# Kernel optimization log

Hardware: AMD Instinct MI355X
Metric: run time of the kernel (lower is better)

## Reference

```python
import jax, jax.numpy as jnp
import numpy as np

N_NODES = 50000
N_EDGES = 800000
H = 128
D = 128
N_LAYERS = 4
N_GRAPHS = 128
NODE_VOCAB = 32
EDGE_VOCAB = 8
BN_EPS = 1e-5


def _bn(h, g, b):
    # BatchNorm1d, training-mode statistics (biased variance), as in the torch module
    m = h.mean(axis=0)
    v = ((h - m) ** 2).mean(axis=0)
    return (h - m) * jax.lax.rsqrt(v + BN_EPS) * g + b


def _gine(x, src, dst, e, eps_l):
    # GINEConv: message = ReLU(x_src + edge_attr), sum-aggregate at dst
    msg = jax.nn.relu(x[src] + e)                      # [E, H]
    aggr = jax.ops.segment_sum(msg, dst, num_segments=N_NODES)
    return (1.0 + eps_l) * x + aggr


def _forward(x_ids, edge_index, batch, edge_attr,
             node_emb, edge_emb, eps,
             init_W1, init_b1, init_g1, init_be1, init_W2, init_b2, init_g2, init_be2,
             mp_W1, mp_g1, mp_be1, mp_W2, mp_g2, mp_be2,
             l1_W1, l1_g1, l1_b1, l1_W2, l1_g2, l1_b2,
             l2_W1, l2_g1, l2_b1, l2_W2, l2_g2, l2_b2,
             fin_W):
    src, dst = edge_index[0], edge_index[1]
    x = node_emb[x_ids]                                # [N, H]
    e = edge_emb[edge_attr]                            # [E, H]
    # initialization conv (Linear layers WITH bias)
    h = _gine(x, src, dst, e, eps[0])
    h = jax.nn.relu(_bn(h @ init_W1 + init_b1, init_g1, init_be1))
    x = jax.nn.relu(_bn(h @ init_W2 + init_b2, init_g2, init_be2))
    # message-passing layers (Linear layers WITHOUT bias)
    for i in range(N_LAYERS):
        h = _gine(x, src, dst, e, eps[1 + i])
        h = jax.nn.relu(_bn(h @ mp_W1[i], mp_g1[i], mp_be1[i]))
        x = jax.nn.relu(_bn(h @ mp_W2[i], mp_g2[i], mp_be2[i]))
    # readout: global_add_pool
    g = jax.ops.segment_sum(x, batch, num_segments=N_GRAPHS)   # [G, H]
    # lin1 (outer F.relu is idempotent; dropout = identity in eval)
    h = jax.nn.relu(_bn(g @ l1_W1, l1_g1, l1_b1))
    h = jax.nn.relu(_bn(h @ l1_W2, l1_g2, l1_b2))
    # lin2
    h = jax.nn.relu(_bn(h @ l2_W1, l2_g1, l2_b1))
    h = jax.nn.relu(_bn(h @ l2_W2, l2_g2, l2_b2))
    return h @ fin_W                                   # [G, 1]


def setup_inputs() -> dict:
    key = jax.random.key(0)
    ks = jax.random.split(key, 20)
    s = 1.0 / np.sqrt(H)
    rn = lambda k, shp, sc: jax.random.normal(k, shp, dtype=jnp.float32) * sc
    return {
        "x_ids": jax.random.randint(ks[0], (N_NODES,), 0, NODE_VOCAB),
        "edge_index": jax.random.randint(ks[1], (2, N_EDGES), 0, N_NODES),
        "batch": jnp.sort(jax.random.randint(ks[2], (N_NODES,), 0, N_GRAPHS)),
        "edge_attr": jax.random.randint(ks[14], (N_EDGES,), 0, EDGE_VOCAB),
        "node_emb": rn(ks[3], (NODE_VOCAB, H), 0.05),
        "edge_emb": rn(ks[4], (EDGE_VOCAB, H), 0.05),
        "eps": jnp.zeros((N_LAYERS + 1,), jnp.float32),
        "init_W1": rn(ks[5], (H, D), s), "init_b1": jnp.zeros((D,)),
        "init_g1": jnp.ones((D,)), "init_be1": jnp.zeros((D,)),
        "init_W2": rn(ks[6], (D, H), s), "init_b2": jnp.zeros((H,)),
        "init_g2": jnp.ones((H,)), "init_be2": jnp.zeros((H,)),
        "mp_W1": rn(ks[7], (N_LAYERS, H, D), s),
        "mp_g1": jnp.ones((N_LAYERS, D)), "mp_be1": jnp.zeros((N_LAYERS, D)),
        "mp_W2": rn(ks[8], (N_LAYERS, D, H), s),
        "mp_g2": jnp.ones((N_LAYERS, H)), "mp_be2": jnp.zeros((N_LAYERS, H)),
        "l1_W1": rn(ks[9], (H, D), s), "l1_g1": jnp.ones((D,)), "l1_b1": jnp.zeros((D,)),
        "l1_W2": rn(ks[10], (D, D), s), "l1_g2": jnp.ones((D,)), "l1_b2": jnp.zeros((D,)),
        "l2_W1": rn(ks[11], (D, D), s), "l2_g1": jnp.ones((D,)), "l2_b1": jnp.zeros((D,)),
        "l2_W2": rn(ks[12], (D, H), s), "l2_g2": jnp.ones((H,)), "l2_b2": jnp.zeros((H,)),
        "fin_W": rn(ks[13], (H, 1), s),
    }


def reference(x_ids, edge_index, batch, edge_attr,
              node_emb, edge_emb, eps,
              init_W1, init_b1, init_g1, init_be1, init_W2, init_b2, init_g2, init_be2,
              mp_W1, mp_g1, mp_be1, mp_W2, mp_g2, mp_be2,
              l1_W1, l1_g1, l1_b1, l1_W2, l1_g2, l1_b2,
              l2_W1, l2_g1, l2_b1, l2_W2, l2_g2, l2_b2,
              fin_W):
    return _forward(x_ids, edge_index, batch, edge_attr,
                    node_emb, edge_emb, eps,
                    init_W1, init_b1, init_g1, init_be1, init_W2, init_b2, init_g2, init_be2,
                    mp_W1, mp_g1, mp_be1, mp_W2, mp_g2, mp_be2,
                    l1_W1, l1_g1, l1_b1, l1_W2, l1_g2, l1_b2,
                    l2_W1, l2_g1, l2_b1, l2_W2, l2_g2, l2_b2,
                    fin_W)
```

## Files before the change

kernel.cpp:

```cpp
#include <hip/hip_runtime.h>

#define NN 50000
#define NE 800000
#define NG 128
#define HD 128
#define NL 4
#define BN_EPS 1e-5f
#define REP 32
#define WP 136
#define NB 392
#define EPB 4096

typedef __attribute__((ext_vector_type(8))) short bf16x8;
typedef __attribute__((ext_vector_type(4))) float f32x4;

__device__ __forceinline__ unsigned short f2bf(float f) {
    unsigned u = __float_as_uint(f);
    u += 0x7FFFu + ((u >> 16) & 1u);
    return (unsigned short)(u >> 16);
}
__device__ __forceinline__ float bfval(unsigned short h) { return __uint_as_float((unsigned)h << 16); }
__device__ __forceinline__ float bflo(unsigned u) { return __uint_as_float(u << 16); }
__device__ __forceinline__ float bfhi(unsigned u) { return __uint_as_float(u & 0xFFFF0000u); }

__device__ __forceinline__ void split2(float a, float b, unsigned& hi, unsigned& lo) {
    unsigned ua = __float_as_uint(a), ub = __float_as_uint(b);
    hi = (ua >> 16) | (ub & 0xFFFF0000u);
    float ra = a - __uint_as_float(ua & 0xFFFF0000u);
    float rb = b - __uint_as_float(ub & 0xFFFF0000u);
    lo = (unsigned)f2bf(ra) | ((unsigned)f2bf(rb) << 16);
}
__device__ __forceinline__ unsigned pack2(float a, float b) {
    return (unsigned)f2bf(a) | ((unsigned)f2bf(b) << 16);
}

__device__ __forceinline__ void bn_pre(const float* SQbase,
                                       const float* gam, const float* bet,
                                       float inv_cnt, int t, float* scs, float* shs) {
    if (gam == nullptr) { scs[t] = 1.f; shs[t] = 0.f; return; }
    float s = 0.f, q = 0.f;
#pragma unroll
    for (int r = 0; r < REP; r++) {
        s += SQbase[r * 256 + t];
        q += SQbase[r * 256 + 128 + t];
    }
    float m = s * inv_cnt;
    float var = fmaxf(fmaf(q, inv_cnt, -m * m), 0.f);
    float inv = rsqrtf(var + BN_EPS);
    float sc = gam[t] * inv;
    scs[t] = sc;
    shs[t] = fmaf(-m, sc, bet[t]);
}

__global__ __launch_bounds__(256) void setup_kernel(const int* __restrict__ ids,
                                                    const float* __restrict__ emb,
                                                    unsigned short* __restrict__ Yb,
                                                    const float* __restrict__ iw1,
                                                    const float* __restrict__ iw2,
                                                    const float* __restrict__ mw1,
                                                    const float* __restrict__ mw2,
                                                    unsigned short* __restrict__ Wh,
                                                    unsigned short* __restrict__ Wl,
                                                    const int* __restrict__ dst,
                                                    int* __restrict__ deg) {
    int b = blockIdx.x, t = threadIdx.x;
    if (b < 3125) {
        int i = b * 256 + t;
        if (i < NN * 16) {
            int node = i >> 4, g = i & 15;
            int id = ids[node];
            const float* p = emb + (size_t)id * HD + 8 * g;
            float4 a = *(const float4*)p;
            float4 bb = *(const float4*)(p + 4);
            uint4 o;
            o.x = pack2(a.x, a.y); o.y = pack2(a.z, a.w);
            o.z = pack2(bb.x, bb.y); o.w = pack2(bb.z, bb.w);
            *(uint4*)(Yb + (size_t)node * HD + 8 * g) = o;
        }
    } else if (b < 3765) {
        int i = (b - 3125) * 256 + t;
        if (i < 163840) {
            int seg = i >> 14, loc = i & 16383;
            float v;
            if (seg == 0)      v = iw1[loc];
            else if (seg == 1) v = iw2[loc];
            else if (seg < 6)  v = mw1[(seg - 2) * 16384 + loc];
            else               v = mw2[(seg - 6) * 16384 + loc];
            int k = loc >> 7, n = loc & 127;
            unsigned short h = f2bf(v);
            float r = v - bfval(h);
            Wh[seg * 16384 + n * 128 + k] = h;
            Wl[seg * 16384 + n * 128 + k] = f2bf(r);
        }
    } else {
        int e = (b - 3765) * 256 + t;
        if (e < NE) atomicAdd(&deg[dst[e]], 1);
    }
}

__global__ __launch_bounds__(256) void ybn_kernel(const float* __restrict__ X,
                                                  const float* __restrict__ SQin,
                                                  const float* __restrict__ gam,
                                                  const float* __restrict__ bet,
                                                  unsigned short* __restrict__ Yb) {
    __shared__ float scs[HD], shs[HD];
    int t = threadIdx.x;
    if (t < HD) bn_pre(SQin, gam, bet, 1.f / NN, t, scs, shs);
    __syncthreads();
    int row = blockIdx.x * 16 + (t >> 4);
    int c8 = (t & 15) * 8;
    if (row < NN) {
        const float* p = X + (size_t)row * HD + c8;
        float4 v0 = *(const float4*)p;
        float4 v1 = *(const float4*)(p + 4);
        float4 s0 = *(const float4*)&scs[c8], s1 = *(const float4*)&scs[c8 + 4];
        float4 h0 = *(const float4*)&shs[c8], h1 = *(const float4*)&shs[c8 + 4];
        float f0 = fmaxf(fmaf(v0.x, s0.x, h0.x), 0.f), f1 = fmaxf(fmaf(v0.y, s0.y, h0.y), 0.f);
        float f2 = fmaxf(fmaf(v0.z, s0.z, h0.z), 0.f), f3 = fmaxf(fmaf(v0.w, s0.w, h0.w), 0.f);
        float f4 = fmaxf(fmaf(v1.x, s1.x, h1.x), 0.f), f5 = fmaxf(fmaf(v1.y, s1.y, h1.y), 0.f);
        float f6 = fmaxf(fmaf(v1.z, s1.z, h1.z), 0.f), f7 = fmaxf(fmaf(v1.w, s1.w, h1.w), 0.f);
        uint4 o;
        o.x = pack2(f0, f1); o.y = pack2(f2, f3);
        o.z = pack2(f4, f5); o.w = pack2(f6, f7);
        *(uint4*)(Yb + (size_t)row * HD + c8) = o;
    }
}

__global__ __launch_bounds__(1024) void scan1_kernel(const int* __restrict__ deg,
                                                     int* __restrict__ rowptr,
                                                     int* __restrict__ blockSum) {
    __shared__ int s[1024];
    int b = blockIdx.x, t = threadIdx.x;
    int i = b * 1024 + t;
    int v = (i < NN) ? deg[i] : 0;
    s[t] = v;
    __syncthreads();
    for (int off = 1; off < 1024; off <<= 1) {
        int u = (t >= off) ? s[t - off] : 0;
        __syncthreads();
        s[t] += u;
        __syncthreads();
    }
    if (i < NN) rowptr[i] = s[t] - v;
    if (t == 1023) blockSum[b] = s[1023];
}

__global__ __launch_bounds__(64) void scan2_kernel(const int* __restrict__ blockSum,
                                                   int* __restrict__ blockOff,
                                                   int* __restrict__ rowptr, int nblocks) {
    int t = threadIdx.x;
    int orig = (t < nblocks) ? blockSum[t] : 0;
    int v = orig;
    for (int off = 1; off < 64; off <<= 1) {
        int u = __shfl_up(v, off, 64);
        if (t >= off) v += u;
    }
    if (t < nblocks) blockOff[t] = v - orig;
    if (t == nblocks - 1) rowptr[NN] = v;
}

__global__ __launch_bounds__(1024) void scan3_kernel(int* __restrict__ rowptr,
                                                     int* __restrict__ cursor,
                                                     const int* __restrict__ blockOff,
                                                     int* __restrict__ bucketCursor) {
    int b = blockIdx.x, t = threadIdx.x;
    int i = b * 1024 + t;
    if (i < NN) {
        int r = rowptr[i] + blockOff[b];
        rowptr[i] = r;
        cursor[i] = r;
        if ((i & 127) == 0) bucketCursor[i >> 7] = r;
    }
}

__global__ __launch_bounds__(256) void bin_kernel(const int* __restrict__ src,
                                                  const int* __restrict__ dst,
                                                  const int* __restrict__ attr,
                                                  int* __restrict__ bucketCursor,
                                                  uint2* __restrict__ ebuf) {
    __shared__ int cnt[512];
    __shared__ int sc[512], sc2[512];
    __shared__ int base[512];
    __shared__ int garr[NB];
    __shared__ int wof[NB];
    __shared__ uint2 stage[EPB];
    int t = threadIdx.x;
    int e0 = blockIdx.x * EPB;
    for (int i = t; i < 512; i += 256) cnt[i] = 0;
    __syncthreads();
    int myb[16]; unsigned myv[16]; int myd[16];
#pragma unroll
    for (int j = 0; j < 16; j++) {
        int e = e0 + t + j * 256;
        if (e < NE) {
            int d = dst[e];
            myd[j] = d;
            myv[j] = (unsigned)src[e] | ((unsigned)attr[e] << 16);
            myb[j] = d >> 7;
            atomicAdd(&cnt[myb[j]], 1);
        } else myb[j] = -1;
    }
    __syncthreads();
    for (int k = t; k < 512; k += 256) sc[k] = cnt[k];
    __syncthreads();
    int* sp = sc; int* dp = sc2;
    for (int off = 1; off < 512; off <<= 1) {
        for (int k = t; k < 512; k += 256) dp[k] = sp[k] + (k >= off ? sp[k - off] : 0);
        __syncthreads();
        int* tmp = sp; sp = dp; dp = tmp;
    }
    for (int k = t; k < 512; k += 256) base[k] = sp[k] - cnt[k];
    int total = sp[511];
    __syncthreads();
    for (int b = t; b < NB; b += 256) {
        wof[b] = 0;
        if (cnt[b] > 0) garr[b] = atomicAdd(&bucketCursor[b], cnt[b]);
    }
    __syncthreads();
#pragma unroll
    for (int j = 0; j < 16; j++) {
        if (myb[j] >= 0) {
            int slot = base[myb[j]] + atomicAdd(&wof[myb[j]], 1);
            stage[slot] = make_uint2(myv[j], (unsigned)myd[j]);
        }
    }
    __syncthreads();
    for (int i = t; i < total; i += 256) {
        uint2 u = stage[i];
        int b = (int)(u.y >> 7);
        ebuf[garr[b] + (i - base[b])] = u;
    }
}

__global__ __launch_bounds__(256) void place_kernel(const uint2* __restrict__ ebuf,
                                                    const int* __restrict__ rowptr,
                                                    int* __restrict__ cursor,
                                                    unsigned* __restrict__ csr) {
    int b = blockIdx.x;
    int n0 = b * 128;
    int n1 = n0 + 128; if (n1 > NN) n1 = NN;
    int es = rowptr[n0], ee = rowptr[n1];
    for (int i = es + threadIdx.x; i < ee; i += 256) {
        uint2 u = ebuf[i];
        int pos = atomicAdd(&cursor[u.y], 1);
        csr[pos] = u.x;
    }
}

__device__ __forceinline__ void gine_acc(const unsigned short* __restrict__ Yb,
                                         const float* __restrict__ elds,
                                         unsigned p, int cq, float mask, float* a) {
    uint4 q = *(const uint4*)(Yb + (size_t)(p & 0xFFFFu) * HD + 8 * cq);
    const float* ep = elds + (p >> 16) * HD + 8 * cq;
    float4 e0 = *(const float4*)ep;
    float4 e1 = *(const float4*)(ep + 4);
    a[0] += mask * fmaxf(bflo(q.x) + e0.x, 0.f);
    a[1] += mask * fmaxf(bfhi(q.x) + e0.y, 0.f);
    a[2] += mask * fmaxf(bflo(q.y) + e0.z, 0.f);
    a[3] += mask * fmaxf(bfhi(q.y) + e0.w, 0.f);
    a[4] += mask * fmaxf(bflo(q.z) + e1.x, 0.f);
    a[5] += mask * fmaxf(bfhi(q.z) + e1.y, 0.f);
    a[6] += mask * fmaxf(bflo(q.w) + e1.z, 0.f);
    a[7] += mask * fmaxf(bfhi(q.w) + e1.w, 0.f);
}

__global__ __launch_bounds__(256) void conv_kernel(const unsigned short* __restrict__ Yb,
                                                   const int* __restrict__ rowptr,
                                                   const unsigned* __restrict__ csr,
                                                   const float* __restrict__ edge_emb,
                                                   const float* __restrict__ eps, int layer,
                                                   unsigned short* __restrict__ Ah,
                                                   unsigned short* __restrict__ Al) {
    __shared__ float elds[8 * HD];
    int t = threadIdx.x;
    ((float4*)elds)[t] = ((const float4*)edge_emb)[t];
    __syncthreads();
    int wave = t >> 6, lane = t & 63;
    int node = blockIdx.x * 4 + wave;
    if (node >= NN) return;
    int sub = lane >> 4, cq = lane & 15;
    int lo = rowptr[node], hi = rowptr[node + 1];
    float a[8];
#pragma unroll
    for (int i = 0; i < 8; i++) a[i] = 0.f;
    for (int base = lo; base < hi; base += 64) {
        unsigned pl = 0;
        int cnt = hi - base; if (cnt > 64) cnt = 64;
        if (base + lane < hi) pl = csr[base + lane];
        int j = 0;
        for (; j + 16 <= cnt; j += 16) {
            unsigned pa = __shfl(pl, j + sub, 64);
            unsigned pb = __shfl(pl, j + 4 + sub, 64);
            unsigned pc = __shfl(pl, j + 8 + sub, 64);
            unsigned pd = __shfl(pl, j + 12 + sub, 64);
            gine_acc(Yb, elds, pa, cq, 1.f, a);
            gine_acc(Yb, elds, pb, cq, 1.f, a);
            gine_acc(Yb, elds, pc, cq, 1.f, a);
            gine_acc(Yb, elds, pd, cq, 1.f, a);
        }
        for (; j + 8 <= cnt; j += 8) {
            unsigned pa = __shfl(pl, j + sub, 64);
            unsigned pb = __shfl(pl, j + 4 + sub, 64);
            gine_acc(Yb, elds, pa, cq, 1.f, a);
            gine_acc(Yb, elds, pb, cq, 1.f, a);
        }
        for (; j < cnt; j += 4) {
            int je = j + sub;
            bool val = (je < cnt);
            unsigned p = __shfl(pl, val ? je : j, 64);
            gine_acc(Yb, elds, p, cq, val ? 1.f : 0.f, a);
        }
    }
#pragma unroll
    for (int i = 0; i < 8; i++) {
        a[i] += __shfl_xor(a[i], 16, 64);
        a[i] += __shfl_xor(a[i], 32, 64);
    }
    if (sub == 0) {
        float g = 1.f + eps[layer];
        uint4 q = *(const uint4*)(Yb + (size_t)node * HD + 8 * cq);
        float o0 = fmaf(g, bflo(q.x), a[0]), o1 = fmaf(g, bfhi(q.x), a[1]);
        float o2 = fmaf(g, bflo(q.y), a[2]), o3 = fmaf(g, bfhi(q.y), a[3]);
        float o4 = fmaf(g, bflo(q.z), a[4]), o5 = fmaf(g, bfhi(q.z), a[5]);
        float o6 = fmaf(g, bflo(q.w), a[6]), o7 = fmaf(g, bfhi(q.w), a[7]);
        uint4 H, L;
        split2(o0, o1, H.x, L.x);
        split2(o2, o3, H.y, L.y);
        split2(o4, o5, H.z, L.z);
        split2(o6, o7, H.w, L.w);
        *(uint4*)(Ah + (size_t)node * HD + 8 * cq) = H;
        *(uint4*)(Al + (size_t)node * HD + 8 * cq) = L;
    }
}

__global__ __launch_bounds__(256) void mm_mfma_pre(const unsigned short* __restrict__ Ah,
                                                   const unsigned short* __restrict__ Al,
                                                   const unsigned short* __restrict__ Wh,
                                                   const unsigned short* __restrict__ Wl,
                                                   const float* __restrict__ bias,
                                                   float* __restrict__ out,
                                                   float* __restrict__ SQout) {
    __shared__ unsigned short WhS[128 * WP];
    __shared__ unsigned short WlS[128 * WP];
    int t = threadIdx.x;
    int rowblk = blockIdx.x;
#pragma unroll
    for (int i = 0; i < 8; i++) {
        int idx = t + i * 256;
        int col = idx >> 4, kk = (idx & 15) * 8;
        *(uint4*)(WhS + col * WP + kk) = *(const uint4*)(Wh + (size_t)col * HD + kk);
        *(uint4*)(WlS + col * WP + kk) = *(const uint4*)(Wl + (size_t)col * HD + kk);
    }
    __syncthreads();
    int w = t >> 6, lane = t & 63;
    int quad = lane >> 4, nl = lane & 15;
    int row0 = rowblk * 128 + w * 32;
    int rA0 = row0 + nl, rA1 = row0 + 16 + nl;
    bool ok0 = rA0 < NN, ok1 = rA1 < NN;
    f32x4 acc[16];
#pragma unroll
    for (int i = 0; i < 16; i++) acc[i] = (f32x4){0.f, 0.f, 0.f, 0.f};
#pragma unroll
    for (int kc = 0; kc < 4; kc++) {
        int k0 = kc * 32 + quad * 8;
        bf16x8 a0h = ok0 ? *(const bf16x8*)(Ah + (size_t)rA0 * HD + k0) : (bf16x8)0;
        bf16x8 a0l = ok0 ? *(const bf16x8*)(Al + (size_t)rA0 * HD + k0) : (bf16x8)0;
        bf16x8 a1h = ok1 ? *(const bf16x8*)(Ah + (size_t)rA1 * HD + k0) : (bf16x8)0;
        bf16x8 a1l = ok1 ? *(const bf16x8*)(Al + (size_t)rA1 * HD + k0) : (bf16x8)0;
#pragma unroll
        for (int c = 0; c < 8; c++) {
            int wof = (c * 16 + nl) * WP + k0;
            bf16x8 bh = *(const bf16x8*)(WhS + wof);
            bf16x8 bl = *(const bf16x8*)(WlS + wof);
            acc[c] = __builtin_amdgcn_mfma_f32_16x16x32_bf16(a0h, bh, acc[c], 0, 0, 0);
            acc[c] = __builtin_amdgcn_mfma_f32_16x16x32_bf16(a0l, bh, acc[c], 0, 0, 0);
            acc[c] = __builtin_amdgcn_mfma_f32_16x16x32_bf16(a0h, bl, acc[c], 0, 0, 0);
            acc[8 + c] = __builtin_amdgcn_mfma_f32_16x16x32_bf16(a1h, bh, acc[8 + c], 0, 0, 0);
            acc[8 + c] = __builtin_amdgcn_mfma_f32_16x16x32_bf16(a1l, bh, acc[8 + c], 0, 0, 0);
            acc[8 + c] = __builtin_amdgcn_mfma_f32_16x16x32_bf16(a1h, bl, acc[8 + c], 0, 0, 0);
        }
    }
    int rep = (blockIdx.x & (REP - 1)) * 256;
#pragma unroll
    for (int h = 0; h < 2; h++) {
        int baserow = row0 + h * 16 + quad * 4;
#pragma unroll
        for (int c = 0; c < 8; c++) {
            int col = c * 16 + nl;
            float bv = bias ? bias[col] : 0.f;
            f32x4 v = acc[h * 8 + c];
            float s = 0.f, qq = 0.f;
#pragma unroll
            for (int r = 0; r < 4; r++) {
                int grow = baserow + r;
                float val = v[r] + bv;
                if (grow < NN) {
                    out[(size_t)grow * HD + col] = val;
                    s += val;
                    qq += val * val;
                }
            }
            s += __shfl_xor(s, 16, 64);  s += __shfl_xor(s, 32, 64);
            qq += __shfl_xor(qq, 16, 64); qq += __shfl_xor(qq, 32, 64);
            if (quad == 0) {
                atomicAdd(&SQout[rep + col], s);
                atomicAdd(&SQout[rep + 128 + col], qq);
            }
        }
    }
}

__global__ __launch_bounds__(256) void mm_mfma_act(const float* __restrict__ A,
                                                   const unsigned short* __restrict__ Wh,
                                                   const unsigned short* __restrict__ Wl,
                                                   const float* __restrict__ bias,
                                                   const float* __restrict__ SQin,
                                                   const float* __restrict__ gam,
                                                   const float* __restrict__ bet,
                                                   float* __restrict__ out,
                                                   float* __restrict__ SQout) {
    __shared__ unsigned short WhS[128 * WP];
    __shared__ unsigned short WlS[128 * WP];
    __shared__ float scs[HD], shs[HD];
    int t = threadIdx.x;
    int rowblk = blockIdx.x;
    if (t < HD) bn_pre(SQin, gam, bet, 1.f / NN, t, scs, shs);
#pragma unroll
    for (int i = 0; i < 8; i++) {
        int idx = t + i * 256;
        int col = idx >> 4, kk = (idx & 15) * 8;
        *(uint4*)(WhS + col * WP + kk) = *(const uint4*)(Wh + (size_t)col * HD + kk);
        *(uint4*)(WlS + col * WP + kk) = *(const uint4*)(Wl + (size_t)col * HD + kk);
    }
    __syncthreads();
    int w = t >> 6, lane = t & 63;
    int quad = lane >> 4, nl = lane & 15;
    int row0 = rowblk * 128 + w * 32;
    int rA0 = row0 + nl, rA1 = row0 + 16 + nl;
    bool ok0 = rA0 < NN, ok1 = rA1 < NN;
    f32x4 acc[16];
#pragma unroll
    for (int i = 0; i < 16; i++) acc[i] = (f32x4){0.f, 0.f, 0.f, 0.f};
#pragma unroll
    for (int kc = 0; kc < 4; kc++) {
        int k0 = kc * 32 + quad * 8;
        float4 s0 = *(const float4*)&scs[k0], s1 = *(const float4*)&scs[k0 + 4];
        float4 t0 = *(const float4*)&shs[k0], t1 = *(const float4*)&shs[k0 + 4];
        bf16x8 a0h, a0l, a1h, a1l;
        {
            float4 v0 = ok0 ? *(const float4*)(A + (size_t)rA0 * HD + k0) : make_float4(0, 0, 0, 0);
            float4 v1 = ok0 ? *(const float4*)(A + (size_t)rA0 * HD + k0 + 4) : make_float4(0, 0, 0, 0);
            float f0 = fmaxf(fmaf(v0.x, s0.x, t0.x), 0.f), f1 = fmaxf(fmaf(v0.y, s0.y, t0.y), 0.f);
            float f2 = fmaxf(fmaf(v0.z, s0.z, t0.z), 0.f), f3 = fmaxf(fmaf(v0.w, s0.w, t0.w), 0.f);
            float f4 = fmaxf(fmaf(v1.x, s1.x, t1.x), 0.f), f5 = fmaxf(fmaf(v1.y, s1.y, t1.y), 0.f);
            float f6 = fmaxf(fmaf(v1.z, s1.z, t1.z), 0.f), f7 = fmaxf(fmaf(v1.w, s1.w, t1.w), 0.f);
            if (!ok0) { f0 = f1 = f2 = f3 = f4 = f5 = f6 = f7 = 0.f; }
            unsigned h0, h1, h2, h3, l0, l1, l2, l3;
            split2(f0, f1, h0, l0); split2(f2, f3, h1, l1);
            split2(f4, f5, h2, l2); split2(f6, f7, h3, l3);
            a0h = __builtin_bit_cast(bf16x8, make_uint4(h0, h1, h2, h3));
            a0l = __builtin_bit_cast(bf16x8, make_uint4(l0, l1, l2, l3));
        }
        {
            float4 v0 = ok1 ? *(const float4*)(A + (size_t)rA1 * HD + k0) : make_float4(0, 0, 0, 0);
            float4 v1 = ok1 ? *(const float4*)(A + (size_t)rA1 * HD + k0 + 4) : make_float4(0, 0, 0, 0);
            float f0 = fmaxf(fmaf(v0.x, s0.x, t0.x), 0.f), f1 = fmaxf(fmaf(v0.y, s0.y, t0.y), 0.f);
            float f2 = fmaxf(fmaf(v0.z, s0.z, t0.z), 0.f), f3 = fmaxf(fmaf(v0.w, s0.w, t0.w), 0.f);
            float f4 = fmaxf(fmaf(v1.x, s1.x, t1.x), 0.f), f5 = fmaxf(fmaf(v1.y, s1.y, t1.y), 0.f);
            float f6 = fmaxf(fmaf(v1.z, s1.z, t1.z), 0.f), f7 = fmaxf(fmaf(v1.w, s1.w, t1.w), 0.f);
            if (!ok1) { f0 = f1 = f2 = f3 = f4 = f5 = f6 = f7 = 0.f; }
            unsigned h0, h1, h2, h3, l0, l1, l2, l3;
            split2(f0, f1, h0, l0); split2(f2, f3, h1, l1);
            split2(f4, f5, h2, l2); split2(f6, f7, h3, l3);
            a1h = __builtin_bit_cast(bf16x8, make_uint4(h0, h1, h2, h3));
            a1l = __builtin_bit_cast(bf16x8, make_uint4(l0, l1, l2, l3));
        }
#pragma unroll
        for (int c = 0; c < 8; c++) {
            int wof = (c * 16 + nl) * WP + k0;
            bf16x8 bh = *(const bf16x8*)(WhS + wof);
            bf16x8 bl = *(const bf16x8*)(WlS + wof);
            acc[c] = __builtin_amdgcn_mfma_f32_16x16x32_bf16(a0h, bh, acc[c], 0, 0, 0);
            acc[c] = __builtin_amdgcn_mfma_f32_16x16x32_bf16(a0l, bh, acc[c], 0, 0, 0);
            acc[c] = __builtin_amdgcn_mfma_f32_16x16x32_bf16(a0h, bl, acc[c], 0, 0, 0);
            acc[8 + c] = __builtin_amdgcn_mfma_f32_16x16x32_bf16(a1h, bh, acc[8 + c], 0, 0, 0);
            acc[8 + c] = __builtin_amdgcn_mfma_f32_16x16x32_bf16(a1l, bh, acc[8 + c], 0, 0, 0);
            acc[8 + c] = __builtin_amdgcn_mfma_f32_16x16x32_bf16(a1h, bl, acc[8 + c], 0, 0, 0);
        }
    }
    int rep = (blockIdx.x & (REP - 1)) * 256;
#pragma unroll
    for (int h = 0; h < 2; h++) {
        int baserow = row0 + h * 16 + quad * 4;
#pragma unroll
        for (int c = 0; c < 8; c++) {
            int col = c * 16 + nl;
            float bv = bias ? bias[col] : 0.f;
            f32x4 v = acc[h * 8 + c];
            float s = 0.f, qq = 0.f;
#pragma unroll
            for (int r = 0; r < 4; r++) {
                int grow = baserow + r;
                float val = v[r] + bv;
                if (grow < NN) {
                    out[(size_t)grow * HD + col] = val;
                    s += val;
                    qq += val * val;
                }
            }
            s += __shfl_xor(s, 16, 64);  s += __shfl_xor(s, 32, 64);
            qq += __shfl_xor(qq, 16, 64); qq += __shfl_xor(qq, 32, 64);
            if (quad == 0) {
                atomicAdd(&SQout[rep + col], s);
                atomicAdd(&SQout[rep + 128 + col], qq);
            }
        }
    }
}

__global__ __launch_bounds__(256) void readout_kernel(const float* __restrict__ x,
                                                      const int* __restrict__ batch,
                                                      const float* __restrict__ SQin,
                                                      const float* __restrict__ gam,
                                                      const float* __restrict__ bet,
                                                      float* __restrict__ gout) {
    __shared__ int bat[256];
    __shared__ float scs[HD], shs[HD];
    int t = threadIdx.x;
    int rq = t >> 5, cq = t & 31;
    int r0 = blockIdx.x * 256;
    int i = r0 + t;
    bat[t] = (i < NN) ? batch[i] : -1;
    if (t < HD) bn_pre(SQin, gam, bet, 1.f / NN, t, scs, shs);
    __syncthreads();
    float4 s4 = *(const float4*)&scs[4 * cq];
    float4 h4 = *(const float4*)&shs[4 * cq];
    float4 acc = make_float4(0.f, 0.f, 0.f, 0.f);
    int gcur = -1;
    for (int j = rq; j < 256; j += 8) {
        int r = r0 + j;
        if (r >= NN) break;
        int g = bat[j];
        if (g != gcur) {
            if (gcur >= 0) {
                atomicAdd(&gout[(size_t)gcur * HD + 4 * cq + 0], acc.x);
                atomicAdd(&gout[(size_t)gcur * HD + 4 * cq + 1], acc.y);
                atomicAdd(&gout[(size_t)gcur * HD + 4 * cq + 2], acc.z);
                atomicAdd(&gout[(size_t)gcur * HD + 4 * cq + 3], acc.w);
            }
            acc = make_float4(0.f, 0.f, 0.f, 0.f);
            gcur = g;
        }
        float4 v = *(const float4*)(x + (size_t)r * HD + 4 * cq);
        acc.x += fmaxf(fmaf(v.x, s4.x, h4.x), 0.f);
        acc.y += fmaxf(fmaf(v.y, s4.y, h4.y), 0.f);
        acc.z += fmaxf(fmaf(v.z, s4.z, h4.z), 0.f);
        acc.w += fmaxf(fmaf(v.w, s4.w, h4.w), 0.f);
    }
    if (gcur >= 0) {
        atomicAdd(&gout[(size_t)gcur * HD + 4 * cq + 0], acc.x);
        atomicAdd(&gout[(size_t)gcur * HD + 4 * cq + 1], acc.y);
        atomicAdd(&gout[(size_t)gcur * HD + 4 * cq + 2], acc.z);
        atomicAdd(&gout[(size_t)gcur * HD + 4 * cq + 3], acc.w);
    }
}

__global__ __launch_bounds__(256) void head_fused(const float* __restrict__ Gp,
                                                  const float* __restrict__ Wa,
                                                  const float* __restrict__ Wb,
                                                  const float* __restrict__ Wc,
                                                  const float* __restrict__ Wd,
                                                  const float* __restrict__ g0,
                                                  const float* __restrict__ b0,
                                                  const float* __restrict__ g1,
                                                  const float* __restrict__ b1,
                                                  const float* __restrict__ g2,
                                                  const float* __restrict__ b2,
                                                  const float* __restrict__ g3,
                                                  const float* __restrict__ b3,
                                                  const float* __restrict__ finW,
                                                  float* __restrict__ out) {
    const int AP = 132;
    __shared__ float A_lds[128 * AP];
    __shared__ unsigned short WhS[128 * WP];
    __shared__ unsigned short WlS[128 * WP];
    __shared__ float colS[HD], colQ[HD], scs[HD], shs[HD];
    int t = threadIdx.x;
    if (t < HD) { colS[t] = 0.f; colQ[t] = 0.f; scs[t] = 1.f; shs[t] = 0.f; }
#pragma unroll
    for (int i = 0; i < 16; i++) {
        int idx = t + i * 256;
        int r = idx >> 5, cq = (idx & 31) * 4;
        *(float4*)&A_lds[r * AP + cq] = *(const float4*)(Gp + (size_t)r * HD + cq);
    }
    int w = t >> 6, lane = t & 63;
    int quad = lane >> 4, nl = lane & 15;
    int row0 = w * 32;
    const float* Ws[4] = {Wa, Wb, Wc, Wd};
    const float* Gs[4] = {g0, g1, g2, g3};
    const float* Bs[4] = {b0, b1, b2, b3};
    for (int s = 0; s < 4; s++) {
        const float* W = Ws[s];
        for (int i = t; i < 4096; i += 256) {
            int k = i >> 5, n = (i & 31) * 4;
            float4 v = *(const float4*)(W + (size_t)k * HD + n);
            unsigned short h0 = f2bf(v.x), h1 = f2bf(v.y), h2 = f2bf(v.z), h3 = f2bf(v.w);
            WhS[(n + 0) * WP + k] = h0; WlS[(n + 0) * WP + k] = f2bf(v.x - bfval(h0));
            WhS[(n + 1) * WP + k] = h1; WlS[(n + 1) * WP + k] = f2bf(v.y - bfval(h1));
            WhS[(n + 2) * WP + k] = h2; WlS[(n + 2) * WP + k] = f2bf(v.z - bfval(h2));
            WhS[(n + 3) * WP + k] = h3; WlS[(n + 3) * WP + k] = f2bf(v.w - bfval(h3));
        }
        __syncthreads();
        f32x4 acc[16];
#pragma unroll
        for (int i = 0; i < 16; i++) acc[i] = (f32x4){0.f, 0.f, 0.f, 0.f};
#pragma unroll
        for (int kc = 0; kc < 4; kc++) {
            int k0 = kc * 32 + quad * 8;
            float4 s0 = *(const float4*)&scs[k0], s1 = *(const float4*)&scs[k0 + 4];
            float4 t0 = *(const float4*)&shs[k0], t1 = *(const float4*)&shs[k0 + 4];
            bf16x8 a0h, a0l, a1h, a1l;
            {
                const float* ap = &A_lds[(row0 + nl) * AP + k0];
                float4 v0 = *(const float4*)ap;
                float4 v1 = *(const float4*)(ap + 4);
                float f0 = fmaxf(fmaf(v0.x, s0.x, t0.x), 0.f), f1 = fmaxf(fmaf(v0.y, s0.y, t0.y), 0.f);
                float f2 = fmaxf(fmaf(v0.z, s0.z, t0.z), 0.f), f3 = fmaxf(fmaf(v0.w, s0.w, t0.w), 0.f);
                float f4 = fmaxf(fmaf(v1.x, s1.x, t1.x), 0.f), f5 = fmaxf(fmaf(v1.y, s1.y, t1.y), 0.f);
                float f6 = fmaxf(fmaf(v1.z, s1.z, t1.z), 0.f), f7 = fmaxf(fmaf(v1.w, s1.w, t1.w), 0.f);
                unsigned h0, h1, h2, h3, l0, l1, l2, l3;
                split2(f0, f1, h0, l0); split2(f2, f3, h1, l1);
                split2(f4, f5, h2, l2); split2(f6, f7, h3, l3);
                a0h = __builtin_bit_cast(bf16x8, make_uint4(h0, h1, h2, h3));
                a0l = __builtin_bit_cast(bf16x8, make_uint4(l0, l1, l2, l3));
            }
            {
                const float* ap = &A_lds[(row0 + 16 + nl) * AP + k0];
                float4 v0 = *(const float4*)ap;
                float4 v1 = *(const float4*)(ap + 4);
                float f0 = fmaxf(fmaf(v0.x, s0.x, t0.x), 0.f), f1 = fmaxf(fmaf(v0.y, s0.y, t0.y), 0.f);
                float f2 = fmaxf(fmaf(v0.z, s0.z, t0.z), 0.f), f3 = fmaxf(fmaf(v0.w, s0.w, t0.w), 0.f);
                float f4 = fmaxf(fmaf(v1.x, s1.x, t1.x), 0.f), f5 = fmaxf(fmaf(v1.y, s1.y, t1.y), 0.f);
                float f6 = fmaxf(fmaf(v1.z, s1.z, t1.z), 0.f), f7 = fmaxf(fmaf(v1.w, s1.w, t1.w), 0.f);
                unsigned h0, h1, h2, h3, l0, l1, l2, l3;
                split2(f0, f1, h0, l0); split2(f2, f3, h1, l1);
                split2(f4, f5, h2, l2); split2(f6, f7, h3, l3);
                a1h = __builtin_bit_cast(bf16x8, make_uint4(h0, h1, h2, h3));
                a1l = __builtin_bit_cast(bf16x8, make_uint4(l0, l1, l2, l3));
            }
#pragma unroll
            for (int c = 0; c < 8; c++) {
                int wof = (c * 16 + nl) * WP + k0;
                bf16x8 bh = *(const bf16x8*)(WhS + wof);
                bf16x8 bl = *(const bf16x8*)(WlS + wof);
                acc[c] = __builtin_amdgcn_mfma_f32_16x16x32_bf16(a0h, bh, acc[c], 0, 0, 0);
                acc[c] = __builtin_amdgcn_mfma_f32_16x16x32_bf16(a0l, bh, acc[c], 0, 0, 0);
                acc[c] = __builtin_amdgcn_mfma_f32_16x16x32_bf16(a0h, bl, acc[c], 0, 0, 0);
                acc[8 + c] = __builtin_amdgcn_mfma_f32_16x16x32_bf16(a1h, bh, acc[8 + c], 0, 0, 0);
                acc[8 + c] = __builtin_amdgcn_mfma_f32_16x16x32_bf16(a1l, bh, acc[8 + c], 0, 0, 0);
                acc[8 + c] = __builtin_amdgcn_mfma_f32_16x16x32_bf16(a1h, bl, acc[8 + c], 0, 0, 0);
            }
        }
        __syncthreads();
#pragma unroll
        for (int h = 0; h < 2; h++) {
            int baserow = row0 + h * 16 + quad * 4;
#pragma unroll
            for (int c = 0; c < 8; c++) {
                int col = c * 16 + nl;
                f32x4 v = acc[h * 8 + c];
                float ss = 0.f, qq = 0.f;
#pragma unroll
                for (int r = 0; r < 4; r++) {
                    float val = v[r];
                    A_lds[(baserow + r) * AP + col] = val;
                    ss += val;
                    qq += val * val;
                }
                ss += __shfl_xor(ss, 16, 64);  ss += __shfl_xor(ss, 32, 64);
                qq += __shfl_xor(qq, 16, 64);  qq += __shfl_xor(qq, 32, 64);
                if (quad == 0) {
                    atomicAdd(&colS[col], ss);
                    atomicAdd(&colQ[col], qq);
                }
            }
        }
        __syncthreads();
        if (t < HD) {
            float m = colS[t] * (1.f / NG);
            float var = fmaxf(fmaf(colQ[t], 1.f / NG, -m * m), 0.f);
            float inv = rsqrtf(var + BN_EPS);
            float sc = Gs[s][t] * inv;
            scs[t] = sc;
            shs[t] = fmaf(-m, sc, Bs[s][t]);
            colS[t] = 0.f;
            colQ[t] = 0.f;
        }
        __syncthreads();
    }
    if (t < HD) {
        float ssum = 0.f;
        for (int c = 0; c < HD; c++) {
            float v = fmaxf(fmaf(A_lds[t * AP + c], scs[c], shs[c]), 0.f);
            ssum += v * finW[c];
        }
        out[t] = ssum;
    }
}

extern "C" void kernel_launch(void* const* d_in, const int* in_sizes, int n_in,
                              void* d_out, int out_size, void* d_ws, size_t ws_size,
                              hipStream_t stream) {
    const int* x_ids = (const int*)d_in[0];
    const int* edge_index = (const int*)d_in[1];
    const int* batch = (const int*)d_in[2];
    const int* edge_attr = (const int*)d_in[3];
    const float* node_emb = (const float*)d_in[4];
    const float* edge_emb = (const float*)d_in[5];
    const float* eps = (const float*)d_in[6];
    const float* init_W1 = (const float*)d_in[7];
    const float* init_b1 = (const float*)d_in[8];
    const float* init_g1 = (const float*)d_in[9];
    const float* init_be1 = (const float*)d_in[10];
    const float* init_W2 = (const float*)d_in[11];
    const float* init_b2 = (const float*)d_in[12];
    const float* init_g2 = (const float*)d_in[13];
    const float* init_be2 = (const float*)d_in[14];
    const float* mp_W1 = (const float*)d_in[15];
    const float* mp_g1 = (const float*)d_in[16];
    const float* mp_be1 = (const float*)d_in[17];
    const float* mp_W2 = (const float*)d_in[18];
    const float* mp_g2 = (const float*)d_in[19];
    const float* mp_be2 = (const float*)d_in[20];
    const float* l1_W1 = (const float*)d_in[21];
    const float* l1_g1 = (const float*)d_in[22];
    const float* l1_b1 = (const float*)d_in[23];
    const float* l1_W2 = (const float*)d_in[24];
    const float* l1_g2 = (const float*)d_in[25];
    const float* l1_b2 = (const float*)d_in[26];
    const float* l2_W1 = (const float*)d_in[27];
    const float* l2_g1 = (const float*)d_in[28];
    const float* l2_b1 = (const float*)d_in[29];
    const float* l2_W2 = (const float*)d_in[30];
    const float* l2_g2 = (const float*)d_in[31];
    const float* l2_b2 = (const float*)d_in[32];
    const float* fin_W = (const float*)d_in[33];

    const int* e_src = edge_index;
    const int* e_dst = edge_index + NE;

    const size_t STG = (size_t)REP * 256;
    float* ws = (float*)d_ws;
    float* X = ws;
    float* Bbuf = X + (size_t)NN * HD;
    unsigned short* Yb = (unsigned short*)Bbuf;
    unsigned short* Ah = (unsigned short*)(Bbuf + (size_t)NN * HD);
    unsigned short* Al = Ah + (size_t)NN * HD;
    float* SQ = (float*)(Al + (size_t)NN * HD);
    float* Gp = SQ + 14 * STG;
    int* deg = (int*)(Gp + NG * HD);
    float* Hp = (float*)(deg + 50048);
    float* Hp2 = Hp + NG * HD;
    int* rowptr = (int*)(Hp2 + NG * HD);
    int* cursor = rowptr + 50048;
    int* blockSum = cursor + 50048;
    int* blockOff = blockSum + 64;
    int* bucketCursor = blockOff + 64;
    unsigned* csr = (unsigned*)(bucketCursor + NB);
    unsigned short* Wh = (unsigned short*)(csr + NE);
    unsigned short* Wl = Wh + 163840;
    uint2* ebuf = (uint2*)(Wl + 163840);
    (void)Hp; (void)Hp2;

    const size_t zero_bytes = (14 * STG + NG * HD) * sizeof(float) + 50048 * sizeof(int);
    hipMemsetAsync(SQ, 0, zero_bytes, stream);

    const int SCAN_BLOCKS = (NN + 1023) / 1024;
    setup_kernel<<<6890, 256, 0, stream>>>(x_ids, node_emb, Yb, init_W1, init_W2, mp_W1,
                                           mp_W2, Wh, Wl, e_dst, deg);
    scan1_kernel<<<SCAN_BLOCKS, 1024, 0, stream>>>(deg, rowptr, blockSum);
    scan2_kernel<<<1, 64, 0, stream>>>(blockSum, blockOff, rowptr, SCAN_BLOCKS);
    scan3_kernel<<<SCAN_BLOCKS, 1024, 0, stream>>>(rowptr, cursor, blockOff, bucketCursor);
    bin_kernel<<<(NE + EPB - 1) / EPB, 256, 0, stream>>>(e_src, e_dst, edge_attr,
                                                         bucketCursor, ebuf);
    place_kernel<<<(NN + 127) / 128, 256, 0, stream>>>(ebuf, rowptr, cursor, csr);

    const int mfma_grid = (NN + 127) / 128;
    const int ybn_grid = (NN + 15) / 16;
    for (int i = 0; i <= NL; i++) {
        const unsigned short* Wh1 = Wh + (size_t)(i == 0 ? 0 : 2 + (i - 1)) * 16384;
        const unsigned short* Wl1 = Wl + (size_t)(i == 0 ? 0 : 2 + (i - 1)) * 16384;
        const unsigned short* Wh2 = Wh + (size_t)(i == 0 ? 1 : 6 + (i - 1)) * 16384;
        const unsigned short* Wl2 = Wl + (size_t)(i == 0 ? 1 : 6 + (i - 1)) * 16384;
        const float* b1 = (i == 0) ? init_b1 : nullptr;
        const float* b2 = (i == 0) ? init_b2 : nullptr;
        const float* g1 = (i == 0) ? init_g1 : mp_g1 + (size_t)(i - 1) * HD;
        const float* be1 = (i == 0) ? init_be1 : mp_be1 + (size_t)(i - 1) * HD;
        const float* gp = (i == 1) ? init_g2 : mp_g2 + (size_t)(i - 2) * HD;
        const float* bp = (i == 1) ? init_be2 : mp_be2 + (size_t)(i - 2) * HD;
        float* Sprev = SQ + (size_t)(2 * i - 1) * STG;
        float* S1 = SQ + (size_t)(2 * i) * STG;
        float* S2 = SQ + (size_t)(2 * i + 1) * STG;

        if (i > 0) ybn_kernel<<<ybn_grid, 256, 0, stream>>>(X, Sprev, gp, bp, Yb);
        conv_kernel<<<(NN + 3) / 4, 256, 0, stream>>>(Yb, rowptr, csr, edge_emb, eps, i, Ah, Al);
        mm_mfma_pre<<<mfma_grid, 256, 0, stream>>>(Ah, Al, Wh1, Wl1, b1, Bbuf, S1);
        mm_mfma_act<<<mfma_grid, 256, 0, stream>>>(Bbuf, Wh2, Wl2, b2, S1, g1, be1, X, S2);
    }

    float* S9 = SQ + 9 * STG;
    readout_kernel<<<(NN + 255) / 256, 256, 0, stream>>>(
        X, batch, S9, mp_g2 + 3 * HD, mp_be2 + 3 * HD, Gp);

    head_fused<<<1, 256, 0, stream>>>(Gp, l1_W1, l1_W2, l2_W1, l2_W2,
                                      l1_g1, l1_b1, l1_g2, l1_b2,
                                      l2_g1, l2_b1, l2_g2, l2_b2,
                                      fin_W, (float*)d_out);
}
```

Before: 791.3 us.

## Widen single-block head kernel to 1024 threads with 2D warp tiling

The single-block MLP head now runs 16 waves instead of 4. Each wave computes a 32x32 output tile instead of a 32x128 strip, so MFMA work is spread over more SIMDs. Weight conversion now writes vectorized packed bf16 hi/lo pairs into LDS instead of scattered 16-bit stores. The final dot product with fin_W is split across 8 lanes per row and combined with shuffles. This targets the serial latency of a one-block tail kernel, at the cost of more threads contending at barriers and for LDS atomics.

Result: faster. 772.7 us (-2.4%).

```diff
diff --git a/kernel.cpp b/kernel.cpp
--- a/kernel.cpp
+++ b/kernel.cpp
@@ -565,21 +565,136 @@
     }
 }
 
-__global__ __launch_bounds__(256) void head_fused(const float* __restrict__ Gp,
-                                                  const float* __restrict__ Wa,
-                                                  const float* __restrict__ Wb,
-                                                  const float* __restrict__ Wc,
-                                                  const float* __restrict__ Wd,
-                                                  const float* __restrict__ g0,
-                                                  const float* __restrict__ b0,
-                                                  const float* __restrict__ g1,
-                                                  const float* __restrict__ b1,
-                                                  const float* __restrict__ g2,
-                                                  const float* __restrict__ b2,
-                                                  const float* __restrict__ g3,
-                                                  const float* __restrict__ b3,
-                                                  const float* __restrict__ finW,
-                                                  float* __restrict__ out) {
+__device__ __forceinline__ void head_stage(const float* __restrict__ W,
+                                           const float* __restrict__ gam,
+                                           const float* __restrict__ bet,
+                                           float* A_lds,
+                                           unsigned short* WhS, unsigned short* WlS,
+                                           float* colS, float* colQ,
+                                           float* scs, float* shs) {
+    const int AP = 132;
+    int t = threadIdx.x;
+#pragma unroll
+    for (int j = 0; j < 2; j++) {
+        int i = t + j * 1024;
+        int n = i & 127, kb = (i >> 7) * 8;
+        unsigned hw[4], lw[4];
+#pragma unroll
+        for (int d = 0; d < 4; d++) {
+            float va = W[(size_t)(kb + 2 * d) * HD + n];
+            float vb = W[(size_t)(kb + 2 * d + 1) * HD + n];
+            split2(va, vb, hw[d], lw[d]);
+        }
+        *(uint4*)(WhS + n * WP + kb) = make_uint4(hw[0], hw[1], hw[2], hw[3]);
+        *(uint4*)(WlS + n * WP + kb) = make_uint4(lw[0], lw[1], lw[2], lw[3]);
+    }
+    __syncthreads();
+    int w = t >> 6, lane = t & 63;
+    int quad = lane >> 4, nl = lane & 15;
+    int row0 = (w >> 2) * 32, col0 = (w & 3) * 32;
+    f32x4 acc[4];
+#pragma unroll
+    for (int i = 0; i < 4; i++) acc[i] = (f32x4){0.f, 0.f, 0.f, 0.f};
+#pragma unroll
+    for (int kc = 0; kc < 4; kc++) {
+        int k0 = kc * 32 + quad * 8;
+        float4 s0 = *(const float4*)&scs[k0], s1 = *(const float4*)&scs[k0 + 4];
+        float4 t0 = *(const float4*)&shs[k0], t1 = *(const float4*)&shs[k0 + 4];
+        bf16x8 a0h, a0l, a1h, a1l;
+        {
+            const float* ap = &A_lds[(row0 + nl) * AP + k0];
+            float4 v0 = *(const float4*)ap;
+            float4 v1 = *(const float4*)(ap + 4);
+            float f0 = fmaxf(fmaf(v0.x, s0.x, t0.x), 0.f), f1 = fmaxf(fmaf(v0.y, s0.y, t0.y), 0.f);
+            float f2 = fmaxf(fmaf(v0.z, s0.z, t0.z), 0.f), f3 = fmaxf(fmaf(v0.w, s0.w, t0.w), 0.f);
+            float f4 = fmaxf(fmaf(v1.x, s1.x, t1.x), 0.f), f5 = fmaxf(fmaf(v1.y, s1.y, t1.y), 0.f);
+            float f6 = fmaxf(fmaf(v1.z, s1.z, t1.z), 0.f), f7 = fmaxf(fmaf(v1.w, s1.w, t1.w), 0.f);
+            unsigned h0, h1, h2, h3, l0, l1, l2, l3;
+            split2(f0, f1, h0, l0); split2(f2, f3, h1, l1);
+            split2(f4, f5, h2, l2); split2(f6, f7, h3, l3);
+            a0h = __builtin_bit_cast(bf16x8, make_uint4(h0, h1, h2, h3));
+            a0l = __builtin_bit_cast(bf16x8, make_uint4(l0, l1, l2, l3));
+        }
+        {
+            const float* ap = &A_lds[(row0 + 16 + nl) * AP + k0];
+            float4 v0 = *(const float4*)ap;
+            float4 v1 = *(const float4*)(ap + 4);
+            float f0 = fmaxf(fmaf(v0.x, s0.x, t0.x), 0.f), f1 = fmaxf(fmaf(v0.y, s0.y, t0.y), 0.f);
+            float f2 = fmaxf(fmaf(v0.z, s0.z, t0.z), 0.f), f3 = fmaxf(fmaf(v0.w, s0.w, t0.w), 0.f);
+            float f4 = fmaxf(fmaf(v1.x, s1.x, t1.x), 0.f), f5 = fmaxf(fmaf(v1.y, s1.y, t1.y), 0.f);
+            float f6 = fmaxf(fmaf(v1.z, s1.z, t1.z), 0.f), f7 = fmaxf(fmaf(v1.w, s1.w, t1.w), 0.f);
+            unsigned h0, h1, h2, h3, l0, l1, l2, l3;
+            split2(f0, f1, h0, l0); split2(f2, f3, h1, l1);
+            split2(f4, f5, h2, l2); split2(f6, f7, h3, l3);
+            a1h = __builtin_bit_cast(bf16x8, make_uint4(h0, h1, h2, h3));
+            a1l = __builtin_bit_cast(bf16x8, make_uint4(l0, l1, l2, l3));
+        }
+#pragma unroll
+        for (int cc = 0; cc < 2; cc++) {
+            int wof = (col0 + cc * 16 + nl) * WP + k0;
+            bf16x8 bh = *(const bf16x8*)(WhS + wof);
+            bf16x8 bl = *(const bf16x8*)(WlS + wof);
+            acc[cc] = __builtin_amdgcn_mfma_f32_16x16x32_bf16(a0h, bh, acc[cc], 0, 0, 0);
+            acc[cc] = __builtin_amdgcn_mfma_f32_16x16x32_bf16(a0l, bh, acc[cc], 0, 0, 0);
+            acc[cc] = __builtin_amdgcn_mfma_f32_16x16x32_bf16(a0h, bl, acc[cc], 0, 0, 0);
+            acc[2 + cc] = __builtin_amdgcn_mfma_f32_16x16x32_bf16(a1h, bh, acc[2 + cc], 0, 0, 0);
+            acc[2 + cc] = __builtin_amdgcn_mfma_f32_16x16x32_bf16(a1l, bh, acc[2 + cc], 0, 0, 0);
+            acc[2 + cc] = __builtin_amdgcn_mfma_f32_16x16x32_bf16(a1h, bl, acc[2 + cc], 0, 0, 0);
+        }
+    }
+    __syncthreads();
+#pragma unroll
+    for (int h = 0; h < 2; h++) {
+        int baserow = row0 + h * 16 + quad * 4;
+#pragma unroll
+        for (int cc = 0; cc < 2; cc++) {
+            int col = col0 + cc * 16 + nl;
+            f32x4 v = acc[h * 2 + cc];
+            float ss = 0.f, qq = 0.f;
+#pragma unroll
+            for (int r = 0; r < 4; r++) {
+                float val = v[r];
+                A_lds[(baserow + r) * AP + col] = val;
+                ss += val;
+                qq += val * val;
+            }
+            ss += __shfl_xor(ss, 16, 64);  ss += __shfl_xor(ss, 32, 64);
+            qq += __shfl_xor(qq, 16, 64);  qq += __shfl_xor(qq, 32, 64);
+            if (quad == 0) {
+                atomicAdd(&colS[col], ss);
+                atomicAdd(&colQ[col], qq);
+            }
+        }
+    }
+    __syncthreads();
+    if (t < HD) {
+        float m = colS[t] * (1.f / NG);
+        float var = fmaxf(fmaf(colQ[t], 1.f / NG, -m * m), 0.f);
+        float inv = rsqrtf(var + BN_EPS);
+        float sc = gam[t] * inv;
+        scs[t] = sc;
+        shs[t] = fmaf(-m, sc, bet[t]);
+        colS[t] = 0.f;
+        colQ[t] = 0.f;
+    }
+    __syncthreads();
+}
+
+__global__ __launch_bounds__(1024) void head_fused(const float* __restrict__ Gp,
+                                                   const float* __restrict__ Wa,
+                                                   const float* __restrict__ Wb,
+                                                   const float* __restrict__ Wc,
+                                                   const float* __restrict__ Wd,
+                                                   const float* __restrict__ g0,
+                                                   const float* __restrict__ b0,
+                                                   const float* __restrict__ g1,
+                                                   const float* __restrict__ b1,
+                                                   const float* __restrict__ g2,
+                                                   const float* __restrict__ b2,
+                                                   const float* __restrict__ g3,
+                                                   const float* __restrict__ b3,
+                                                   const float* __restrict__ finW,
+                                                   float* __restrict__ out) {
     const int AP = 132;
     __shared__ float A_lds[128 * AP];
     __shared__ unsigned short WhS[128 * WP];
@@ -588,124 +703,27 @@
     int t = threadIdx.x;
     if (t < HD) { colS[t] = 0.f; colQ[t] = 0.f; scs[t] = 1.f; shs[t] = 0.f; }
 #pragma unroll
-    for (int i = 0; i < 16; i++) {
-        int idx = t + i * 256;
+    for (int i = 0; i < 4; i++) {
+        int idx = t + i * 1024;
         int r = idx >> 5, cq = (idx & 31) * 4;
         *(float4*)&A_lds[r * AP + cq] = *(const float4*)(Gp + (size_t)r * HD + cq);
     }
-    int w = t >> 6, lane = t & 63;
-    int quad = lane >> 4, nl = lane & 15;
-    int row0 = w * 32;
-    const float* Ws[4] = {Wa, Wb, Wc, Wd};
-    const float* Gs[4] = {g0, g1, g2, g3};
-    const float* Bs[4] = {b0, b1, b2, b3};
-    for (int s = 0; s < 4; s++) {
-        const float* W = Ws[s];
-        for (int i = t; i < 4096; i += 256) {
-            int k = i >> 5, n = (i & 31) * 4;
-            float4 v = *(const float4*)(W + (size_t)k * HD + n);
-            unsigned short h0 = f2bf(v.x), h1 = f2bf(v.y), h2 = f2bf(v.z), h3 = f2bf(v.w);
-            WhS[(n + 0) * WP + k] = h0; WlS[(n + 0) * WP + k] = f2bf(v.x - bfval(h0));
-            WhS[(n + 1) * WP + k] = h1; WlS[(n + 1) * WP + k] = f2bf(v.y - bfval(h1));
-            WhS[(n + 2) * WP + k] = h2; WlS[(n + 2) * WP + k] = f2bf(v.z - bfval(h2));
-            WhS[(n + 3) * WP + k] = h3; WlS[(n + 3) * WP + k] = f2bf(v.w - bfval(h3));
-        }
-        __syncthreads();
-        f32x4 acc[16];
-#pragma unroll
-        for (int i = 0; i < 16; i++) acc[i] = (f32x4){0.f, 0.f, 0.f, 0.f};
-#pragma unroll
-        for (int kc = 0; kc < 4; kc++) {
-            int k0 = kc * 32 + quad * 8;
-            float4 s0 = *(const float4*)&scs[k0], s1 = *(const float4*)&scs[k0 + 4];
-            float4 t0 = *(const float4*)&shs[k0], t1 = *(const float4*)&shs[k0 + 4];
-            bf16x8 a0h, a0l, a1h, a1l;
-            {
-                const float* ap = &A_lds[(row0 + nl) * AP + k0];
-                float4 v0 = *(const float4*)ap;
-                float4 v1 = *(const float4*)(ap + 4);
-                float f0 = fmaxf(fmaf(v0.x, s0.x, t0.x), 0.f), f1 = fmaxf(fmaf(v0.y, s0.y, t0.y), 0.f);
-                float f2 = fmaxf(fmaf(v0.z, s0.z, t0.z), 0.f), f3 = fmaxf(fmaf(v0.w, s0.w, t0.w), 0.f);
-                float f4 = fmaxf(fmaf(v1.x, s1.x, t1.x), 0.f), f5 = fmaxf(fmaf(v1.y, s1.y, t1.y), 0.f);
-                float f6 = fmaxf(fmaf(v1.z, s1.z, t1.z), 0.f), f7 = fmaxf(fmaf(v1.w, s1.w, t1.w), 0.f);
-                unsigned h0, h1, h2, h3, l0, l1, l2, l3;
-                split2(f0, f1, h0, l0); split2(f2, f3, h1, l1);
-                split2(f4, f5, h2, l2); split2(f6, f7, h3, l3);
-                a0h = __builtin_bit_cast(bf16x8, make_uint4(h0, h1, h2, h3));
-                a0l = __builtin_bit_cast(bf16x8, make_uint4(l0, l1, l2, l3));
-            }
-            {
-                const float* ap = &A_lds[(row0 + 16 + nl) * AP + k0];
-                float4 v0 = *(const float4*)ap;
-                float4 v1 = *(const float4*)(ap + 4);
-                float f0 = fmaxf(fmaf(v0.x, s0.x, t0.x), 0.f), f1 = fmaxf(fmaf(v0.y, s0.y, t0.y), 0.f);
-                float f2 = fmaxf(fmaf(v0.z, s0.z, t0.z), 0.f), f3 = fmaxf(fmaf(v0.w, s0.w, t0.w), 0.f);
-                float f4 = fmaxf(fmaf(v1.x, s1.x, t1.x), 0.f), f5 = fmaxf(fmaf(v1.y, s1.y, t1.y), 0.f);
-                float f6 = fmaxf(fmaf(v1.z, s1.z, t1.z), 0.f), f7 = fmaxf(fmaf(v1.w, s1.w, t1.w), 0.f);
-                unsigned h0, h1, h2, h3, l0, l1, l2, l3;
-                split2(f0, f1, h0, l0); split2(f2, f3, h1, l1);
-                split2(f4, f5, h2, l2); split2(f6, f7, h3, l3);
-                a1h = __builtin_bit_cast(bf16x8, make_uint4(h0, h1, h2, h3));
-                a1l = __builtin_bit_cast(bf16x8, make_uint4(l0, l1, l2, l3));
-            }
-#pragma unroll
-            for (int c = 0; c < 8; c++) {
-                int wof = (c * 16 + nl) * WP + k0;
-                bf16x8 bh = *(const bf16x8*)(WhS + wof);
-                bf16x8 bl = *(const bf16x8*)(WlS + wof);
-                acc[c] = __builtin_amdgcn_mfma_f32_16x16x32_bf16(a0h, bh, acc[c], 0, 0, 0);
-                acc[c] = __builtin_amdgcn_mfma_f32_16x16x32_bf16(a0l, bh, acc[c], 0, 0, 0);
-                acc[c] = __builtin_amdgcn_mfma_f32_16x16x32_bf16(a0h, bl, acc[c], 0, 0, 0);
-                acc[8 + c] = __builtin_amdgcn_mfma_f32_16x16x32_bf16(a1h, bh, acc[8 + c], 0, 0, 0);
-                acc[8 + c] = __builtin_amdgcn_mfma_f32_16x16x32_bf16(a1l, bh, acc[8 + c], 0, 0, 0);
-                acc[8 + c] = __builtin_amdgcn_mfma_f32_16x16x32_bf16(a1h, bl, acc[8 + c], 0, 0, 0);
-            }
-        }
-        __syncthreads();
-#pragma unroll
-        for (int h = 0; h < 2; h++) {
-            int baserow = row0 + h * 16 + quad * 4;
-#pragma unroll
-            for (int c = 0; c < 8; c++) {
-                int col = c * 16 + nl;
-                f32x4 v = acc[h * 8 + c];
-                float ss = 0.f, qq = 0.f;
-#pragma unroll
-                for (int r = 0; r < 4; r++) {
-                    float val = v[r];
-                    A_lds[(baserow + r) * AP + col] = val;
-                    ss += val;
-                    qq += val * val;
-                }
-                ss += __shfl_xor(ss, 16, 64);  ss += __shfl_xor(ss, 32, 64);
-                qq += __shfl_xor(qq, 16, 64);  qq += __shfl_xor(qq, 32, 64);
-                if (quad == 0) {
-                    atomicAdd(&colS[col], ss);
-                    atomicAdd(&colQ[col], qq);
-                }
-            }
-        }
-        __syncthreads();
-        if (t < HD) {
-            float m = colS[t] * (1.f / NG);
-            float var = fmaxf(fmaf(colQ[t], 1.f / NG, -m * m), 0.f);
-            float inv = rsqrtf(var + BN_EPS);
-            float sc = Gs[s][t] * inv;
-            scs[t] = sc;
-            shs[t] = fmaf(-m, sc, Bs[s][t]);
-            colS[t] = 0.f;
-            colQ[t] = 0.f;
-        }
-        __syncthreads();
-    }
-    if (t < HD) {
-        float ssum = 0.f;
-        for (int c = 0; c < HD; c++) {
-            float v = fmaxf(fmaf(A_lds[t * AP + c], scs[c], shs[c]), 0.f);
-            ssum += v * finW[c];
-        }
-        out[t] = ssum;
-    }
+    head_stage(Wa, g0, b0, A_lds, WhS, WlS, colS, colQ, scs, shs);
+    head_stage(Wb, g1, b1, A_lds, WhS, WlS, colS, colQ, scs, shs);
+    head_stage(Wc, g2, b2, A_lds, WhS, WlS, colS, colQ, scs, shs);
+    head_stage(Wd, g3, b3, A_lds, WhS, WlS, colS, colQ, scs, shs);
+    int r = t >> 3, g = t & 7;
+    float ssum = 0.f;
+#pragma unroll
+    for (int j = 0; j < 16; j++) {
+        int c = g * 16 + j;
+        float v = fmaxf(fmaf(A_lds[r * AP + c], scs[c], shs[c]), 0.f);
+        ssum += v * finW[c];
+    }
+    ssum += __shfl_xor(ssum, 1, 64);
+    ssum += __shfl_xor(ssum, 2, 64);
+    ssum += __shfl_xor(ssum, 4, 64);
+    if (g == 0) out[r] = ssum;
 }
 
 extern "C" void kernel_launch(void* const* d_in, const int* in_sizes, int n_in,
@@ -812,8 +830,8 @@
     readout_kernel<<<(NN + 255) / 256, 256, 0, stream>>>(
         X, batch, S9, mp_g2 + 3 * HD, mp_be2 + 3 * HD, Gp);
 
-    head_fused<<<1, 256, 0, stream>>>(Gp, l1_W1, l1_W2, l2_W1, l2_W2,
-                                      l1_g1, l1_b1, l1_g2, l1_b2,
-                                      l2_g1, l2_b1, l2_g2, l2_b2,
-                                      fin_W, (float*)d_out);
-}
+    head_fused<<<1, 1024, 0, stream>>>(Gp, l1_W1, l1_W2, l2_W1, l2_W2,
+                                       l1_g1, l1_b1, l1_g2, l1_b2,
+                                       l2_g1, l2_b1, l2_g2, l2_b2,
+                                       fin_W, (float*)d_out);
+}
```
